# Performance work log

Hardware: AMD Instinct MI355X
Metric: run time of the kernel (lower is better)

Reference implementation:

```python
import jax, jax.numpy as jnp
import numpy as np

D_MODEL = 1024
D_K = 1024
D_V = 1024
N_HEAD = 16
EPS = 1e-5
BS, N_TOK = 2, 2048


def setup_inputs() -> dict:
    key = jax.random.key(0)
    ks = jax.random.split(key, 12)
    s = 0.02
    q = jax.random.normal(ks[0], (BS, N_TOK, D_MODEL), jnp.float32)
    k = jax.random.normal(ks[1], (BS, N_TOK, D_MODEL), jnp.float32)
    v = jax.random.normal(ks[2], (BS, N_TOK, D_MODEL), jnp.float32)
    return {
        "q": q, "k": k, "v": v,
        "gamma": jnp.ones((D_MODEL,), jnp.float32),
        "beta": jnp.zeros((D_MODEL,), jnp.float32),
        "Wq": jax.random.normal(ks[3], (D_MODEL, D_K), jnp.float32) * s,
        "bq": jnp.zeros((D_K,), jnp.float32),
        "Wk": jax.random.normal(ks[4], (D_MODEL, D_K), jnp.float32) * s,
        "bk": jnp.zeros((D_K,), jnp.float32),
        "Wv": jax.random.normal(ks[5], (D_MODEL, D_V), jnp.float32) * s,
        "bv": jnp.zeros((D_V,), jnp.float32),
        "Wo": jax.random.normal(ks[6], (D_V, D_MODEL), jnp.float32) * s,
        "bo": jnp.zeros((D_MODEL,), jnp.float32),
    }


def reference(q, k, v, gamma, beta, Wq, bq, Wk, bk, Wv, bv, Wo, bo):
    # NOTE: original module ignores k, v args; self-attention over q.
    bs, n_tok, d_m = q.shape
    d_h = D_K // N_HEAD
    temper = float(np.sqrt(d_h))

    # LayerNorm1d over d_model
    mu = jnp.mean(q, axis=-1, keepdims=True)
    var = jnp.var(q, axis=-1, keepdims=True)
    h = (q - mu) / jnp.sqrt(var + EPS) * gamma + beta

    # projections; head split = chunk along feature dim -> [bs, H, T, d_h]
    qh = (h @ Wq + bq).reshape(bs, n_tok, N_HEAD, d_h).transpose(0, 2, 1, 3)
    kh = (h @ Wk + bk).reshape(bs, n_tok, N_HEAD, d_h).transpose(0, 2, 1, 3)
    vh = jax.nn.relu(h @ Wv + bv).reshape(bs, n_tok, N_HEAD, d_h).transpose(0, 2, 1, 3)

    scores = jnp.einsum('bhqd,bhkd->bhqk', qh, kh) / temper
    # dropout before softmax in train mode; identity in eval (deterministic ref)
    attn = jax.nn.softmax(scores, axis=-1)
    o = jnp.einsum('bhqk,bhkd->bhqd', attn, vh)  # [bs, H, T, d_h]

    # faithful to torch: view(bs, n_tok, -1) with NO head transpose (head-major merge)
    merged = o.reshape(bs, n_tok, N_HEAD * d_h)
    out = merged @ Wo + bo + q  # proj + residual
    return out
```

## Files before the change

### kernel.cpp

```cpp
#include <hip/hip_runtime.h>

typedef __bf16 bf16;
typedef __bf16 bf16x8 __attribute__((ext_vector_type(8)));
typedef __bf16 bf16x4 __attribute__((ext_vector_type(4)));
typedef float  f32x4  __attribute__((ext_vector_type(4)));
typedef float  f32x16 __attribute__((ext_vector_type(16)));
typedef unsigned int u32;
typedef u32 u32x4 __attribute__((ext_vector_type(4)));

#define AS1U(p) ((const __attribute__((address_space(1))) unsigned int*)(p))
#define AS3U(p) ((__attribute__((address_space(3))) unsigned int*)(p))

static __device__ __forceinline__ u32 pack2(float a, float b) {
    unsigned short ua = __builtin_bit_cast(unsigned short, (bf16)a);
    unsigned short ub = __builtin_bit_cast(unsigned short, (bf16)b);
    return (u32)ua | ((u32)ub << 16);
}

__global__ void prep_kernel(const float* __restrict__ q,
                            const float* __restrict__ gamma,
                            const float* __restrict__ beta,
                            bf16* __restrict__ h,
                            const float* __restrict__ W0, const float* __restrict__ W1,
                            const float* __restrict__ W2, const float* __restrict__ W3,
                            bf16* __restrict__ D0, bf16* __restrict__ D1,
                            bf16* __restrict__ D2, bf16* __restrict__ D3) {
    __shared__ float tile[32][33];
    __shared__ float ssum[4], ssum2[4];
    const int blk = blockIdx.x;
    const int t = threadIdx.x;
    if (blk < 4096) {
        const float* xr = q + (size_t)blk * 1024;
        float4 v = ((const float4*)xr)[t];
        float s  = v.x + v.y + v.z + v.w;
        float s2 = v.x * v.x + v.y * v.y + v.z * v.z + v.w * v.w;
#pragma unroll
        for (int m = 1; m < 64; m <<= 1) {
            s  += __shfl_xor(s, m, 64);
            s2 += __shfl_xor(s2, m, 64);
        }
        const int wid = t >> 6, lane = t & 63;
        if (lane == 0) { ssum[wid] = s; ssum2[wid] = s2; }
        __syncthreads();
        s  = ssum[0] + ssum[1] + ssum[2] + ssum[3];
        s2 = ssum2[0] + ssum2[1] + ssum2[2] + ssum2[3];
        const float mu  = s * (1.f / 1024.f);
        const float var = s2 * (1.f / 1024.f) - mu * mu;
        const float rs  = rsqrtf(var + 1e-5f);
        float4 g = ((const float4*)gamma)[t];
        float4 b = ((const float4*)beta)[t];
        bf16x4 o;
        o[0] = (bf16)((v.x - mu) * rs * g.x + b.x);
        o[1] = (bf16)((v.y - mu) * rs * g.y + b.y);
        o[2] = (bf16)((v.z - mu) * rs * g.z + b.z);
        o[3] = (bf16)((v.w - mu) * rs * g.w + b.w);
        ((bf16x4*)(h + (size_t)blk * 1024))[t] = o;
    } else {
        const int z = blk - 4096;
        const float* W; bf16* D;
        switch (z >> 10) {
            case 0: W = W0; D = D0; break;
            case 1: W = W1; D = D1; break;
            case 2: W = W2; D = D2; break;
            default: W = W3; D = D3; break;
        }
        const int bi = (z & 1023) >> 5, bj = z & 31;
        const int tx = t & 31, ty = t >> 5;
#pragma unroll
        for (int i = 0; i < 4; i++) {
            tile[ty + i * 8][tx] = W[(size_t)(bi * 32 + ty + i * 8) * 1024 + bj * 32 + tx];
        }
        __syncthreads();
#pragma unroll
        for (int i = 0; i < 4; i++) {
            D[(size_t)(bj * 32 + ty + i * 8) * 1024 + bi * 32 + tx] =
                (bf16)tile[tx][ty + i * 8];
        }
    }
}

__global__ __launch_bounds__(256, 2)
void gemm0_kernel(const bf16* __restrict__ A, const bf16* __restrict__ BT,
                  bf16* __restrict__ Cb,
                  const float* __restrict__ b0, const float* __restrict__ b1,
                  const float* __restrict__ b2, bf16* __restrict__ Vt) {
    __shared__ char lds[32768];
    const int tid = threadIdx.x;
    const int lane = tid & 63, wave = tid >> 6;
    const int wr = wave >> 1, wc = wave & 1;
    const int bid0 = blockIdx.y * 24 + blockIdx.x;
    const int bid = (bid0 & 7) * 96 + (bid0 >> 3);
    const int tileN = (bid % 24) * 128;
    const int tileM = (bid / 24) * 128;
    const int row16 = lane & 15, g = lane >> 4;

    auto stage = [&](int T, int slot) {
        const int kt = T * 32;
        char* ab = lds + slot * 8192;
        char* bb = lds + 16384 + slot * 8192;
#pragma unroll
        for (int i = 0; i < 2; i++) {
            const int c = tid + i * 256;
            const int r = c >> 2, cbyte = (c & 3) * 16;
            const char* ga = (const char*)(A + (size_t)(tileM + r) * 1024 + kt) + cbyte;
            __builtin_amdgcn_global_load_lds(AS1U(ga), AS3U(ab + c * 16), 16, 0, 0);
            const char* gb = (const char*)(BT + (size_t)(tileN + r) * 1024 + kt) + cbyte;
            __builtin_amdgcn_global_load_lds(AS1U(gb), AS3U(bb + c * 16), 16, 0, 0);
        }
    };

    f32x4 acc[4][4] = {};
    stage(0, 0);

#pragma unroll 1
    for (int T = 0; T < 32; ++T) {
        asm volatile("s_waitcnt vmcnt(0)" ::: "memory");
        __builtin_amdgcn_s_barrier();
        asm volatile("" ::: "memory");
        if (T < 31) stage(T + 1, (T + 1) & 1);
        const char* Ab = lds + (T & 1) * 8192;
        const char* Bb = lds + 16384 + (T & 1) * 8192;
        bf16x8 af[4], bfr[4];
#pragma unroll
        for (int m = 0; m < 4; m++)
            af[m] = *(const bf16x8*)(Ab + (size_t)(wr * 64 + m * 16 + row16) * 64 + g * 16);
#pragma unroll
        for (int n = 0; n < 4; n++)
            bfr[n] = *(const bf16x8*)(Bb + (size_t)(wc * 64 + n * 16 + row16) * 64 + g * 16);
        __builtin_amdgcn_s_setprio(1);
#pragma unroll
        for (int m = 0; m < 4; m++)
#pragma unroll
            for (int n = 0; n < 4; n++)
                acc[m][n] = __builtin_amdgcn_mfma_f32_16x16x32_bf16(af[m], bfr[n],
                                                                   acc[m][n], 0, 0, 0);
        __builtin_amdgcn_s_setprio(0);
    }

    __syncthreads();
    char* ep = lds + wave * 8192;
    const bool isV = (tileN >= 2048);
    if (!isV) {
#pragma unroll
        for (int n = 0; n < 4; n++) {
            const int cl = n * 16 + row16;
            const int gc = tileN + wc * 64 + cl;
            const float bias = gc < 1024 ? b0[gc] : b1[gc - 1024];
            const float scl = gc < 1024 ? 0.18033688011112042f : 1.f;
#pragma unroll
            for (int m = 0; m < 4; m++)
#pragma unroll
                for (int j = 0; j < 4; j++) {
                    const int rl = m * 16 + g * 4 + j;
                    const float v = (acc[m][n][j] + bias) * scl;
                    *(bf16*)(ep + rl * 128 + ((cl * 2) ^ ((rl & 7) << 4))) = (bf16)v;
                }
        }
    } else {
#pragma unroll
        for (int n = 0; n < 4; n++) {
            const int dl = n * 16 + row16;
            const float bias = b2[(tileN - 2048) + wc * 64 + dl];
#pragma unroll
            for (int m = 0; m < 4; m++)
#pragma unroll
                for (int j = 0; j < 4; j++) {
                    const int tl = m * 16 + g * 4 + j;
                    const float v = fmaxf(acc[m][n][j] + bias, 0.f);
                    *(bf16*)(ep + dl * 128 + ((tl * 2) ^ ((dl & 7) << 4))) = (bf16)v;
                }
        }
    }
    asm volatile("s_waitcnt lgkmcnt(0)" ::: "memory");
    __builtin_amdgcn_sched_barrier(0);
    if (!isV) {
#pragma unroll
        for (int it = 0; it < 8; it++) {
            const int rl = (lane >> 3) + it * 8;
            const bf16x8 vrow = *(const bf16x8*)(ep + rl * 128 +
                                                 (((lane & 7) * 16) ^ ((rl & 7) << 4)));
            const int gr = tileM + wr * 64 + rl;
            const int gc = tileN + wc * 64 + (lane & 7) * 8;
            *(bf16x8*)&Cb[(size_t)gr * 3072 + gc] = vrow;
        }
    } else {
        const int bb = tileM >> 11;
        const int tbase = (tileM & 2047) + wr * 64 + (lane & 7) * 8;
#pragma unroll
        for (int it = 0; it < 8; it++) {
            const int dl = (lane >> 3) + it * 8;
            const bf16x8 vrow = *(const bf16x8*)(ep + dl * 128 +
                                                 (((lane & 7) * 16) ^ ((dl & 7) << 4)));
            const int gd = (tileN - 2048) + wc * 64 + dl;
            const int hh = gd >> 6, dd = gd & 63;
            *(bf16x8*)&Vt[(((size_t)bb * 16 + hh) * 64 + dd) * 2048 + tbase] = vrow;
        }
    }
}

__global__ void gemm1_kernel(const bf16* __restrict__ A, const bf16* __restrict__ BT,
                             float* __restrict__ Cf, const float* __restrict__ bo,
                             const float* __restrict__ resid) {
    __shared__ bf16 Asm[128][32];
    __shared__ bf16 Bsm[128][32];
    const int tid = threadIdx.x;
    const int lane = tid & 63, wave = tid >> 6;
    const int wr = wave >> 1, wc = wave & 1;
    const int nwg = gridDim.x * gridDim.y;
    const int bid0 = blockIdx.y * gridDim.x + blockIdx.x;
    const int bid = (bid0 & 7) * (nwg >> 3) + (bid0 >> 3);
    const int tileN = (bid % gridDim.x) * 128;
    const int tileM = (bid / gridDim.x) * 128;
    const int row16 = lane & 15, g = lane >> 4;

    f32x4 acc[4][4] = {};

    for (int kt = 0; kt < 1024; kt += 32) {
#pragma unroll
        for (int i = 0; i < 2; i++) {
            int c = tid + i * 256;
            int r = c >> 2, cb = (c & 3) * 16;
            const char* g_ = (const char*)(A + (size_t)(tileM + r) * 1024 + kt) + cb;
            __builtin_amdgcn_global_load_lds(AS1U(g_), AS3U((char*)&Asm[0][0] + c * 16), 16, 0, 0);
        }
#pragma unroll
        for (int i = 0; i < 2; i++) {
            int c = tid + i * 256;
            int r = c >> 2, cb = (c & 3) * 16;
            const char* g_ = (const char*)(BT + (size_t)(tileN + r) * 1024 + kt) + cb;
            __builtin_amdgcn_global_load_lds(AS1U(g_), AS3U((char*)&Bsm[0][0] + c * 16), 16, 0, 0);
        }
        __syncthreads();
        bf16x8 af[4], bfr[4];
#pragma unroll
        for (int m = 0; m < 4; m++)
            af[m] = *(const bf16x8*)&Asm[wr * 64 + m * 16 + row16][g * 8];
#pragma unroll
        for (int n = 0; n < 4; n++)
            bfr[n] = *(const bf16x8*)&Bsm[wc * 64 + n * 16 + row16][g * 8];
#pragma unroll
        for (int m = 0; m < 4; m++)
#pragma unroll
            for (int n = 0; n < 4; n++)
                acc[m][n] = __builtin_amdgcn_mfma_f32_16x16x32_bf16(af[m], bfr[n],
                                                                   acc[m][n], 0, 0, 0);
        __syncthreads();
    }
    __shared__ float Epf[4][64][66];
    float* ep = &Epf[wave][0][0];
#pragma unroll
    for (int n = 0; n < 4; n++) {
        const int cl = n * 16 + row16;
        const float bias = bo[tileN + wc * 64 + cl];
#pragma unroll
        for (int m = 0; m < 4; m++)
#pragma unroll
            for (int j = 0; j < 4; j++) {
                const int rl = m * 16 + g * 4 + j;
                ep[rl * 66 + cl] = acc[m][n][j] + bias;
            }
    }
    asm volatile("s_waitcnt lgkmcnt(0)" ::: "memory");
    __builtin_amdgcn_sched_barrier(0);
    const int rl0 = lane >> 4;
    const int cl0 = (lane & 15) * 4;
#pragma unroll
    for (int it = 0; it < 16; it++) {
        const int rl = rl0 + it * 4;
        float4 v = *(const float4*)&ep[rl * 66 + cl0];
        const int gr = tileM + wr * 64 + rl;
        const int gc = tileN + wc * 64 + cl0;
        const float4 rv = *(const float4*)&resid[(size_t)gr * 1024 + gc];
        v.x += rv.x; v.y += rv.y; v.z += rv.z; v.w += rv.w;
        *(float4*)&Cf[(size_t)gr * 1024 + gc] = v;
    }
}

__global__ __launch_bounds__(512, 4)
void attn_kernel(const bf16* __restrict__ qkv, const bf16* __restrict__ Vt,
                 bf16* __restrict__ Obuf) {
    const int bid = blockIdx.x;
    const int swz = (bid & 7) * 64 + (bid >> 3);
    const int bh = swz >> 4, qt = swz & 15;
    const int b = bh >> 4, h = bh & 15;
    const int qbase = qt * 128;
    const int tid = threadIdx.x;
    const int lane = tid & 63, wv = tid >> 6;
    const int half = wv >> 2, qw = wv & 3;
    const int c = lane & 31, p = lane >> 5;

    __shared__ bf16 Kl[2][2][64][64];
    __shared__ bf16 Vl[2][2][64][64];

    const bf16* qrow = qkv + (size_t)(b * 2048 + qbase + qw * 32 + c) * 3072 + h * 64;
    bf16x8 qf[4];
#pragma unroll
    for (int ch = 0; ch < 4; ch++)
        qf[ch] = *(const bf16x8*)(qrow + ch * 16 + p * 8);

    const char* kgbase = (const char*)(qkv + (size_t)b * 2048 * 3072 + 1024 + h * 64)
                         + (size_t)(half * 1024) * 6144;
    const char* vgbase = (const char*)(Vt + (size_t)bh * 64 * 2048) + half * 2048;
    const int ht = tid & 255;
    const char* kgp[2]; const char* vgp[2]; int ldo[2];
#pragma unroll
    for (int i = 0; i < 2; i++) {
        const int cc = ht + i * 256;
        const int srow = cc >> 3;
        const int scol = ((cc & 7) * 16) ^ ((srow & 7) << 4);
        kgp[i] = kgbase + (size_t)srow * 6144 + scol;
        vgp[i] = vgbase + (size_t)srow * 4096 + scol;
        ldo[i] = cc * 16;
    }
    char* kldb = (char*)&Kl[half][0][0][0];
    char* vldb = (char*)&Vl[half][0][0][0];

    auto stage = [&](int t, int slot) {
        const size_t ko = (size_t)t * (64 * 6144);
        const size_t vo = (size_t)t * 128;
        const int sb = slot * 8192;
#pragma unroll
        for (int i = 0; i < 2; i++) {
            __builtin_amdgcn_global_load_lds(AS1U(kgp[i] + ko), AS3U(kldb + sb + ldo[i]), 16, 0, 0);
            __builtin_amdgcn_global_load_lds(AS1U(vgp[i] + vo), AS3U(vldb + sb + ldo[i]), 16, 0, 0);
        }
    };

    f32x16 accO[2] = {};
    f32x16 accL = {};
    const f32x16 z16 = {};
    const u32 one2 = 0x3F803F80u;
    const u32x4 onesw = {one2, one2, one2, one2};
    const bf16x8 onesf = __builtin_bit_cast(bf16x8, onesw);

    auto compute = [&](int slot) {
        const char* Kb = (const char*)&Kl[half][slot][0][0];
        const char* Vb = (const char*)&Vl[half][slot][0][0];
#pragma unroll
        for (int cc = 0; cc < 2; cc++) {
            const int tok = cc * 32 + c;
            const bf16x8 kf0 = *(const bf16x8*)(Kb + tok * 128 + ((p * 16) ^ ((tok & 7) << 4)));
            f32x16 accT = __builtin_amdgcn_mfma_f32_32x32x16_bf16(kf0, qf[0], z16, 0, 0, 0);
#pragma unroll
            for (int ch = 1; ch < 4; ch++) {
                const bf16x8 kf = *(const bf16x8*)(Kb + tok * 128 +
                                                   ((ch * 32 + p * 16) ^ ((tok & 7) << 4)));
                accT = __builtin_amdgcn_mfma_f32_32x32x16_bf16(kf, qf[ch], accT, 0, 0, 0);
            }
            float pv[16];
#pragma unroll
            for (int r = 0; r < 16; r++) pv[r] = exp2f(accT[r]);
            u32 k01 = pack2(pv[0], pv[1]),  k23 = pack2(pv[2], pv[3]);
            u32 k45 = pack2(pv[4], pv[5]),  k67 = pack2(pv[6], pv[7]);
            u32 k89 = pack2(pv[8], pv[9]),  kab = pack2(pv[10], pv[11]);
            u32 kcd = pack2(pv[12], pv[13]), kef = pack2(pv[14], pv[15]);
            asm("v_permlane32_swap_b32 %0, %1" : "+v"(k45), "+v"(k01));
            asm("v_permlane32_swap_b32 %0, %1" : "+v"(k67), "+v"(k23));
            asm("v_permlane32_swap_b32 %0, %1" : "+v"(kcd), "+v"(k89));
            asm("v_permlane32_swap_b32 %0, %1" : "+v"(kef), "+v"(kab));
            u32x4 w0w = {k01, k23, k45, k67};
            u32x4 w1w = {k89, kab, kcd, kef};
            const bf16x8 pf0 = __builtin_bit_cast(bf16x8, w0w);
            const bf16x8 pf1 = __builtin_bit_cast(bf16x8, w1w);
            accL = __builtin_amdgcn_mfma_f32_32x32x16_bf16(pf0, onesf, accL, 0, 0, 0);
            accL = __builtin_amdgcn_mfma_f32_32x32x16_bf16(pf1, onesf, accL, 0, 0, 0);
#pragma unroll
            for (int dc = 0; dc < 2; dc++) {
                const int rd = dc * 32 + c;
                const int sw = (rd & 7) << 4;
                const bf16x8 vf0 = *(const bf16x8*)(Vb + rd * 128 + ((cc * 64 + p * 16) ^ sw));
                const bf16x8 vf1 = *(const bf16x8*)(Vb + rd * 128 + ((cc * 64 + 32 + p * 16) ^ sw));
                accO[dc] = __builtin_amdgcn_mfma_f32_32x32x16_bf16(pf0, vf0, accO[dc], 0, 0, 0);
                accO[dc] = __builtin_amdgcn_mfma_f32_32x32x16_bf16(pf1, vf1, accO[dc], 0, 0, 0);
            }
        }
    };

#define KV_SYNC() do { \
        asm volatile("s_waitcnt vmcnt(0)" ::: "memory"); \
        __builtin_amdgcn_s_barrier(); \
        asm volatile("" ::: "memory"); \
    } while (0)

    stage(0, 0);
#pragma unroll 1
    for (int t = 0; t < 14; t += 2) {
        KV_SYNC(); stage(t + 1, 1); compute(0);
        KV_SYNC(); stage(t + 2, 0); compute(1);
    }
    KV_SYNC(); stage(15, 1); compute(0);
    KV_SYNC(); compute(1);
#undef KV_SYNC

    __syncthreads();
    float* ex = (float*)&Kl[0][0][0][0];
    const int xb = (qw * 64 + lane) * 49;
    if (half) {
#pragma unroll
        for (int dc = 0; dc < 2; dc++)
#pragma unroll
            for (int r = 0; r < 16; r++) ex[xb + dc * 16 + r] = accO[dc][r];
#pragma unroll
        for (int r = 0; r < 16; r++) ex[xb + 32 + r] = accL[r];
    }
    __syncthreads();
    if (!half) {
#pragma unroll
        for (int dc = 0; dc < 2; dc++)
#pragma unroll
            for (int r = 0; r < 16; r++) accO[dc][r] += ex[xb + dc * 16 + r];
#pragma unroll
        for (int r = 0; r < 16; r++) accL[r] += ex[xb + 32 + r];
        bf16* ob = Obuf + ((size_t)bh * 2048 + qbase + qw * 32) * 64;
#pragma unroll
        for (int r = 0; r < 16; r++) {
            const float inv = 1.f / accL[r];
            const int row = (r & 3) + 8 * (r >> 2) + 4 * p;
            ob[(size_t)row * 64 + c]      = (bf16)(accO[0][r] * inv);
            ob[(size_t)row * 64 + 32 + c] = (bf16)(accO[1][r] * inv);
        }
    }
}

extern "C" void kernel_launch(void* const* d_in, const int* in_sizes, int n_in,
                              void* d_out, int out_size, void* d_ws, size_t ws_size,
                              hipStream_t stream) {
    const float* q     = (const float*)d_in[0];
    const float* gamma = (const float*)d_in[3];
    const float* beta  = (const float*)d_in[4];
    const float* Wq    = (const float*)d_in[5];
    const float* bq    = (const float*)d_in[6];
    const float* Wk    = (const float*)d_in[7];
    const float* bk    = (const float*)d_in[8];
    const float* Wv    = (const float*)d_in[9];
    const float* bv    = (const float*)d_in[10];
    const float* Wo    = (const float*)d_in[11];
    const float* bo    = (const float*)d_in[12];
    float* out = (float*)d_out;

    char* ws = (char*)d_ws;
    bf16* h     = (bf16*)(ws);
    bf16* WcatT = (bf16*)(ws + (8u << 20));
    bf16* WoT   = (bf16*)(ws + (14u << 20));
    bf16* qkv   = (bf16*)(ws + (16u << 20));
    bf16* Obuf  = (bf16*)(ws + (40u << 20));
    bf16* Vtb   = (bf16*)(ws + (48u << 20));

    prep_kernel<<<8192, 256, 0, stream>>>(q, gamma, beta, h,
                                          Wq, Wk, Wv, Wo,
                                          WcatT, WcatT + (size_t)1024 * 1024,
                                          WcatT + (size_t)2048 * 1024, WoT);

    gemm0_kernel<<<dim3(24, 32), 256, 0, stream>>>(h, WcatT, qkv, bq, bk, bv, Vtb);

    attn_kernel<<<512, 512, 0, stream>>>(qkv, Vtb, Obuf);

    gemm1_kernel<<<dim3(8, 32), 256, 0, stream>>>(Obuf, WoT, out, bo, q);
}
```

Baseline: 127.2 us.

## Triple-buffer LDS prefetch in both GEMMs; pipeline the output projection GEMM

Moves the QKV projection GEMM from a double-buffered to a triple-buffered LDS pipeline that prefetches two K-tiles ahead and waits with a partial vmcnt. Rewrites the output-projection GEMM, which previously loaded, synced and computed with no overlap, to use the same three-slot async prefetch with a single barrier per step and raised MFMA priority. Its epilogue scratch now reuses the staging LDS. The aim is to hide global load latency behind MFMA work, at the cost of more LDS per block, which may limit how many blocks fit on a CU.

```diff
diff --git a/kernel.cpp b/kernel.cpp
--- a/kernel.cpp
+++ b/kernel.cpp
@@ -84,7 +84,7 @@
                   bf16* __restrict__ Cb,
                   const float* __restrict__ b0, const float* __restrict__ b1,
                   const float* __restrict__ b2, bf16* __restrict__ Vt) {
-    __shared__ char lds[32768];
+    __shared__ char lds[49152];
     const int tid = threadIdx.x;
     const int lane = tid & 63, wave = tid >> 6;
     const int wr = wave >> 1, wc = wave & 1;
@@ -97,7 +97,7 @@
     auto stage = [&](int T, int slot) {
         const int kt = T * 32;
         char* ab = lds + slot * 8192;
-        char* bb = lds + 16384 + slot * 8192;
+        char* bb = lds + 24576 + slot * 8192;
 #pragma unroll
         for (int i = 0; i < 2; i++) {
             const int c = tid + i * 256;
@@ -111,15 +111,18 @@
 
     f32x4 acc[4][4] = {};
     stage(0, 0);
+    stage(1, 1);
 
 #pragma unroll 1
     for (int T = 0; T < 32; ++T) {
-        asm volatile("s_waitcnt vmcnt(0)" ::: "memory");
+        if (T < 31) { asm volatile("s_waitcnt vmcnt(4)" ::: "memory"); }
+        else        { asm volatile("s_waitcnt vmcnt(0)" ::: "memory"); }
         __builtin_amdgcn_s_barrier();
         asm volatile("" ::: "memory");
-        if (T < 31) stage(T + 1, (T + 1) & 1);
-        const char* Ab = lds + (T & 1) * 8192;
-        const char* Bb = lds + 16384 + (T & 1) * 8192;
+        if (T < 30) stage(T + 2, (T + 2) % 3);
+        const int sl = T % 3;
+        const char* Ab = lds + sl * 8192;
+        const char* Bb = lds + 24576 + sl * 8192;
         bf16x8 af[4], bfr[4];
 #pragma unroll
         for (int m = 0; m < 4; m++)
@@ -198,11 +201,11 @@
     }
 }
 
-__global__ void gemm1_kernel(const bf16* __restrict__ A, const bf16* __restrict__ BT,
-                             float* __restrict__ Cf, const float* __restrict__ bo,
-                             const float* __restrict__ resid) {
-    __shared__ bf16 Asm[128][32];
-    __shared__ bf16 Bsm[128][32];
+__global__ __launch_bounds__(256, 2)
+void gemm1_kernel(const bf16* __restrict__ A, const bf16* __restrict__ BT,
+                  float* __restrict__ Cf, const float* __restrict__ bo,
+                  const float* __restrict__ resid) {
+    __shared__ char lds[67584];
     const int tid = threadIdx.x;
     const int lane = tid & 63, wave = tid >> 6;
     const int wr = wave >> 1, wc = wave & 1;
@@ -213,41 +216,54 @@
     const int tileM = (bid / gridDim.x) * 128;
     const int row16 = lane & 15, g = lane >> 4;
 
+    auto stage = [&](int T, int slot) {
+        const int kt = T * 32;
+        char* ab = lds + slot * 8192;
+        char* bb = lds + 24576 + slot * 8192;
+#pragma unroll
+        for (int i = 0; i < 2; i++) {
+            const int c = tid + i * 256;
+            const int r = c >> 2, cbyte = (c & 3) * 16;
+            const char* ga = (const char*)(A + (size_t)(tileM + r) * 1024 + kt) + cbyte;
+            __builtin_amdgcn_global_load_lds(AS1U(ga), AS3U(ab + c * 16), 16, 0, 0);
+            const char* gb = (const char*)(BT + (size_t)(tileN + r) * 1024 + kt) + cbyte;
+            __builtin_amdgcn_global_load_lds(AS1U(gb), AS3U(bb + c * 16), 16, 0, 0);
+        }
+    };
+
     f32x4 acc[4][4] = {};
-
-    for (int kt = 0; kt < 1024; kt += 32) {
-#pragma unroll
-        for (int i = 0; i < 2; i++) {
-            int c = tid + i * 256;
-            int r = c >> 2, cb = (c & 3) * 16;
-            const char* g_ = (const char*)(A + (size_t)(tileM + r) * 1024 + kt) + cb;
-            __builtin_amdgcn_global_load_lds(AS1U(g_), AS3U((char*)&Asm[0][0] + c * 16), 16, 0, 0);
-        }
-#pragma unroll
-        for (int i = 0; i < 2; i++) {
-            int c = tid + i * 256;
-            int r = c >> 2, cb = (c & 3) * 16;
-            const char* g_ = (const char*)(BT + (size_t)(tileN + r) * 1024 + kt) + cb;
-            __builtin_amdgcn_global_load_lds(AS1U(g_), AS3U((char*)&Bsm[0][0] + c * 16), 16, 0, 0);
-        }
-        __syncthreads();
+    stage(0, 0);
+    stage(1, 1);
+
+#pragma unroll 1
+    for (int T = 0; T < 32; ++T) {
+        if (T < 31) { asm volatile("s_waitcnt vmcnt(4)" ::: "memory"); }
+        else        { asm volatile("s_waitcnt vmcnt(0)" ::: "memory"); }
+        __builtin_amdgcn_s_barrier();
+        asm volatile("" ::: "memory");
+        if (T < 30) stage(T + 2, (T + 2) % 3);
+        const int sl = T % 3;
+        const char* Ab = lds + sl * 8192;
+        const char* Bb = lds + 24576 + sl * 8192;
         bf16x8 af[4], bfr[4];
 #pragma unroll
         for (int m = 0; m < 4; m++)
-            af[m] = *(const bf16x8*)&Asm[wr * 64 + m * 16 + row16][g * 8];
+            af[m] = *(const bf16x8*)(Ab + (size_t)(wr * 64 + m * 16 + row16) * 64 + g * 16);
 #pragma unroll
         for (int n = 0; n < 4; n++)
-            bfr[n] = *(const bf16x8*)&Bsm[wc * 64 + n * 16 + row16][g * 8];
+            bfr[n] = *(const bf16x8*)(Bb + (size_t)(wc * 64 + n * 16 + row16) * 64 + g * 16);
+        __builtin_amdgcn_s_setprio(1);
 #pragma unroll
         for (int m = 0; m < 4; m++)
 #pragma unroll
             for (int n = 0; n < 4; n++)
                 acc[m][n] = __builtin_amdgcn_mfma_f32_16x16x32_bf16(af[m], bfr[n],
                                                                    acc[m][n], 0, 0, 0);
-        __syncthreads();
-    }
-    __shared__ float Epf[4][64][66];
-    float* ep = &Epf[wave][0][0];
+        __builtin_amdgcn_s_setprio(0);
+    }
+
+    __syncthreads();
+    float* ep = (float*)lds + (size_t)wave * 64 * 66;
 #pragma unroll
     for (int n = 0; n < 4; n++) {
         const int cl = n * 16 + row16;
```

Measured after the change: 125.1 us. About the same (-1.7%).
